# Kernel optimization log

Measured on AMD Instinct MI355X. Metric: run time of the kernel, lower is better.

Reference implementation:

```python
import jax, jax.numpy as jnp
import numpy as np

B_SZ, L, H, P = 4, 4096, 1024, 1024
R_MIN, R_MAX, MAX_PHASE = 0.0, 1.0, 6.28


def setup_inputs() -> dict:
    key = jax.random.key(0)
    ks = jax.random.split(key, 8)
    inputs = jax.random.normal(ks[0], (B_SZ, L, H), dtype=jnp.float32)
    # LRU-style init for nu_log/theta_log (keeps |lambda| < 1 so scan is stable)
    u1 = jax.random.uniform(ks[1], (P,))
    nu = -0.5 * jnp.log(u1 * (R_MAX**2 - R_MIN**2) + R_MIN**2)
    nu_log = jnp.log(nu)
    u2 = jax.random.uniform(ks[2], (P,))
    theta_log = jnp.log(MAX_PHASE * u2)
    # variance_scaling(0.5,'fan_out','normal') for B; (1.0,'fan_out','normal') for C
    B_re = jax.random.normal(ks[3], (P, H)) * jnp.sqrt(0.5 / P)
    B_im = jax.random.normal(ks[4], (P, H)) * jnp.sqrt(0.5 / P)
    C_re = jax.random.normal(ks[5], (H, P)) * jnp.sqrt(1.0 / H)
    C_im = jax.random.normal(ks[6], (H, P)) * jnp.sqrt(1.0 / H)
    D = jax.random.normal(ks[7], (H,))
    diag_lambda = jnp.exp(-jnp.exp(nu_log) + 1j * jnp.exp(theta_log))
    gamma_log = jnp.log(jnp.sqrt(1.0 - jnp.abs(diag_lambda) ** 2))
    return {
        "inputs": inputs,
        "nu_log": nu_log.astype(jnp.float32),
        "theta_log": theta_log.astype(jnp.float32),
        "B_re": B_re.astype(jnp.float32),
        "B_im": B_im.astype(jnp.float32),
        "C_re": C_re.astype(jnp.float32),
        "C_im": C_im.astype(jnp.float32),
        "D": D.astype(jnp.float32),
        "gamma_log": gamma_log.astype(jnp.float32),
    }


def reference(inputs, nu_log, theta_log, B_re, B_im, C_re, C_im, D, gamma_log):
    batch_size, input_length, _ = inputs.shape
    Lambda = jnp.exp(-jnp.exp(nu_log) + 1j * jnp.exp(theta_log))  # [P] complex
    Bmat = B_re + 1j * B_im                                        # [P,H]
    Cmat = C_re + 1j * C_im                                        # [H,P]
    gamma = jnp.exp(gamma_log)                                     # [P]
    B_norm = Bmat * gamma[:, None]

    def apply_step(elem_i, elem_j):
        a_i, bu_i = elem_i
        a_j, bu_j = elem_j
        return (a_j * a_i, a_j * bu_i + bu_j)

    Ls = jnp.broadcast_to(Lambda, (batch_size, input_length, Lambda.shape[0]))
    Bu = jnp.einsum('ph,blh->blp', B_norm, inputs.astype(B_norm.dtype))
    _, xs = jax.lax.associative_scan(apply_step, (Ls, Bu), axis=1)
    Cx = jnp.einsum('hp,blp->blh', Cmat, xs).real
    Du = D * inputs
    return Cx + Du
```

## Files before the change

kernel.cpp:

```cpp
#include <hip/hip_runtime.h>
#include <cstdint>
#include <cstddef>

#define MDIM 16384
#define HDIM 1024
#define PDIM 1024
#define LSEQ 4096
#define BSZ  4
#define CHUNK 64
#define NCHUNK 64
#define NBU  2048

typedef float   floatx4  __attribute__((ext_vector_type(4)));
typedef __bf16  bf16x8   __attribute__((ext_vector_type(8)));
typedef unsigned short u16;
typedef unsigned short u16x8 __attribute__((ext_vector_type(8)));

__device__ __forceinline__ u16 f2bf(float f) {
    union { float f; uint32_t u; } v; v.f = f;
    return (u16)((v.u + 0x7fffu + ((v.u >> 16) & 1u)) >> 16);
}
__device__ __forceinline__ float bfu2f(uint32_t bits16) {
    union { float f; uint32_t u; } v; v.u = bits16 << 16; return v.f;
}
__device__ __forceinline__ bf16x8 ldfrag(const u16* p) {
    return __builtin_bit_cast(bf16x8, *(const u16x8*)p);
}
__device__ __forceinline__ void gload16(const u16* g, u16* l) {
    __builtin_amdgcn_global_load_lds(
        (const __attribute__((address_space(1))) uint32_t*)g,
        (__attribute__((address_space(3))) uint32_t*)l, 16, 0, 0);
}

#define BARRIER() do { \
    asm volatile("" ::: "memory"); \
    __builtin_amdgcn_sched_barrier(0); \
    __builtin_amdgcn_s_barrier(); \
    __builtin_amdgcn_sched_barrier(0); \
    asm volatile("" ::: "memory"); \
} while (0)

#define WAITV(N_) do { \
    __builtin_amdgcn_sched_barrier(0); \
    asm volatile("s_waitcnt vmcnt(" #N_ ")" ::: "memory"); \
    __builtin_amdgcn_sched_barrier(0); \
} while (0)

template<int MH>
__device__ __forceinline__ void ldA(const u16* buf, int aBase, int c0, int c1,
                                    bf16x8 (&aF)[4][2]) {
    #pragma unroll
    for (int mf = 0; mf < 4; ++mf) {
        const u16* p = buf + aBase + (MH * 4 + mf) * 1024;
        aF[mf][0] = ldfrag(p + c0);
        aF[mf][1] = ldfrag(p + c1);
    }
}
template<int NH>
__device__ __forceinline__ void ldB(const u16* buf, int bBase, int c0, int c1,
                                    bf16x8 (&bF)[2][2]) {
    #pragma unroll
    for (int j = 0; j < 2; ++j) {
        const u16* p = buf + bBase + (NH * 2 + j) * 1024;
        bF[j][0] = ldfrag(p + c0);
        bF[j][1] = ldfrag(p + c1);
    }
}
template<int MH, int NH>
__device__ __forceinline__ void doMFMA(bf16x8 (&aF)[4][2], bf16x8 (&bF)[2][2],
                                       floatx4 (&acc)[8][4]) {
    __builtin_amdgcn_s_setprio(1);
    #pragma unroll
    for (int s = 0; s < 2; ++s)
        #pragma unroll
        for (int mf = 0; mf < 4; ++mf)
            #pragma unroll
            for (int j = 0; j < 2; ++j)
                acc[MH * 4 + mf][NH * 2 + j] =
                    __builtin_amdgcn_mfma_f32_16x16x32_bf16(
                        aF[mf][s], bF[j][s], acc[MH * 4 + mf][NH * 2 + j],
                        0, 0, 0);
    __builtin_amdgcn_s_setprio(0);
}

template<int KD>
__device__ __forceinline__ void gemm256_core(
    const u16* __restrict__ A, const u16* __restrict__ B,
    int m0, int n0, u16* smem, floatx4 (&acc)[8][4])
{
    const int tid  = threadIdx.x;
    const int wave = tid >> 6, lane = tid & 63;
    const int lrow = lane & 15, lq = lane >> 4;
    const int wm = wave >> 2, wn = wave & 3;
    const int axr = lrow & 7;
    const int c0 = (lq ^ axr) * 8;
    const int c1 = ((4 + lq) ^ axr) * 8;
    const int aBase = (wm * 128 + lrow) * 64;
    const int bBase = (wn * 64  + lrow) * 64;
    const int srow = tid >> 3;
    const int schk = (tid & 7) ^ (srow & 7);
    const u16* aptr = A + (size_t)(m0 + srow) * KD + schk * 8;
    const u16* bptr = B + (size_t)(n0 + srow) * KD + schk * 8;
    u16* const sA0 = smem;
    u16* const sB0 = smem + 16384;
    u16* const sA1 = smem + 32768;
    u16* const sB1 = smem + 49152;
    const int lw = wave * 512;

    bf16x8 aF[4][2], bF[2][2];

    #pragma unroll
    for (int i = 0; i < 4; ++i) {
        gload16(aptr + (size_t)i * 64 * KD, sA0 + i * 4096 + lw);
        gload16(bptr + (size_t)i * 64 * KD, sB0 + i * 4096 + lw);
    }
    WAITV(0);
    BARRIER();

    #define STG(i_, k_, dA_, dB_) do { \
        gload16(aptr + (size_t)(i_) * 64 * KD + (k_), (dA_) + (i_) * 4096 + lw); \
        gload16(bptr + (size_t)(i_) * 64 * KD + (k_), (dB_) + (i_) * 4096 + lw); \
    } while (0)

    for (int k = 0; k < KD; k += 128) {
        const int k1 = k + 64, k2 = k + 128;
        STG(0, k1, sA1, sB1);
        WAITV(2);
        BARRIER();
        ldA<0>(sA0, aBase, c0, c1, aF);
        ldB<0>(sB0, bBase, c0, c1, bF);
        doMFMA<0, 0>(aF, bF, acc);
        BARRIER();
        ldB<1>(sB0, bBase, c0, c1, bF);
        STG(1, k1, sA1, sB1);
        BARRIER();
        doMFMA<0, 1>(aF, bF, acc);
        BARRIER();
        ldA<1>(sA0, aBase, c0, c1, aF);
        STG(2, k1, sA1, sB1);
        BARRIER();
        doMFMA<1, 1>(aF, bF, acc);
        BARRIER();
        ldB<0>(sB0, bBase, c0, c1, bF);
        STG(3, k1, sA1, sB1);
        BARRIER();
        doMFMA<1, 0>(aF, bF, acc);
        BARRIER();

        if (k2 < KD) { STG(0, k2, sA0, sB0); WAITV(2); } else { WAITV(0); }
        BARRIER();
        ldA<0>(sA1, aBase, c0, c1, aF);
        ldB<0>(sB1, bBase, c0, c1, bF);
        doMFMA<0, 0>(aF, bF, acc);
        BARRIER();

        ldB<1>(sB1, bBase, c0, c1, bF);
        if (k2 < KD) STG(1, k2, sA0, sB0);
        BARRIER();
        doMFMA<0, 1>(aF, bF, acc);
        BARRIER();

        ldA<1>(sA1, aBase, c0, c1, aF);
        if (k2 < KD) STG(2, k2, sA0, sB0);
        BARRIER();
        doMFMA<1, 1>(aF, bF, acc);
        BARRIER();

        ldB<0>(sB1, bBase, c0, c1, bF);
        if (k2 < KD) STG(3, k2, sA0, sB0);
        BARRIER();
        doMFMA<1, 0>(aF, bF, acc);
        BARRIER();
    }
    #undef STG
}

__global__ __launch_bounds__(512, 2) void gemm_bu_k(
    const u16* __restrict__ A, const u16* __restrict__ B, u16* __restrict__ O)
{
    __shared__ __align__(16) u16 smem[65536];
    floatx4 acc[8][4] = {};
    const int d = blockIdx.x;
    const int xcd = d & 7, s = d >> 3;
    const int m0 = (xcd * 8 + (s >> 3)) * 256;
    const int n0 = (s & 7) * 256;
    gemm256_core<HDIM>(A, B, m0, n0, smem, acc);

    const int tid = threadIdx.x, wave = tid >> 6, lane = tid & 63;
    const int lrow = lane & 15, lq = lane >> 4;
    const int wm = wave >> 2, wn = wave & 3;
    u16* lwp = smem + wave * 4096;
    #pragma unroll
    for (int mh = 0; mh < 2; ++mh) {
        #pragma unroll
        for (int mfl = 0; mfl < 4; ++mfl)
            #pragma unroll
            for (int nf = 0; nf < 4; ++nf)
                #pragma unroll
                for (int r = 0; r < 4; ++r) {
                    int rowl = mfl * 16 + lq * 4 + r;
                    int cpos = (nf * 2 + (lrow >> 3)) ^ (rowl & 7);
                    lwp[rowl * 64 + cpos * 8 + (lrow & 7)] =
                        f2bf(acc[mh * 4 + mfl][nf][r]);
                }
        int grow = m0 + wm * 128 + mh * 64 + lane;
        #pragma unroll
        for (int j = 0; j < 8; ++j) {
            int cpos = j ^ (lane & 7);
            *(u16x8*)(O + (size_t)grow * NBU + n0 + wn * 64 + j * 8) =
                *(const u16x8*)(lwp + lane * 64 + cpos * 8);
        }
    }
}

__global__ __launch_bounds__(512, 2) void gemm_out_k(
    const u16* __restrict__ A, const u16* __restrict__ B,
    const float* __restrict__ Dv, const u16* __restrict__ Ubf,
    float* __restrict__ O)
{
    __shared__ __align__(16) u16 smem[65536];
    floatx4 acc[8][4] = {};
    const int d = blockIdx.x;
    const int xcd = d & 7, s = d >> 3;
    const int m0 = (xcd * 8 + (s >> 2)) * 256;
    const int n0 = (s & 3) * 256;
    gemm256_core<NBU>(A, B, m0, n0, smem, acc);

    const int tid = threadIdx.x, wave = tid >> 6, lane = tid & 63;
    const int lrow = lane & 15, lq = lane >> 4;
    const int wm = wave >> 2, wn = wave & 3;
    #pragma unroll
    for (int nf = 0; nf < 4; ++nf) {
        int col = n0 + wn * 64 + nf * 16 + lrow;
        float dval = Dv[col];
        #pragma unroll
        for (int mf = 0; mf < 8; ++mf)
            #pragma unroll
            for (int r = 0; r < 4; ++r) {
                int row = m0 + wm * 128 + mf * 16 + lq * 4 + r;
                size_t o = (size_t)row * HDIM + col;
                O[o] = acc[mf][nf][r] + dval * bfu2f(Ubf[o]);
            }
    }
}

__global__ __launch_bounds__(256) void prep_all(
    const float* __restrict__ U, u16* __restrict__ Ubf,
    const float* __restrict__ Bre, const float* __restrict__ Bim,
    const float* __restrict__ gamma_log, u16* __restrict__ Bcomb,
    const float* __restrict__ Cre, const float* __restrict__ Cim,
    u16* __restrict__ Bcbf)
{
    const int bid = blockIdx.x;
    if (bid < 8192) {
        size_t i = ((size_t)bid * 256 + threadIdx.x) * 8;
        float4 a = *(const float4*)(U + i);
        float4 b = *(const float4*)(U + i + 4);
        u16x8 w;
        w[0]=f2bf(a.x); w[1]=f2bf(a.y); w[2]=f2bf(a.z); w[3]=f2bf(a.w);
        w[4]=f2bf(b.x); w[5]=f2bf(b.y); w[6]=f2bf(b.z); w[7]=f2bf(b.w);
        *(u16x8*)(Ubf + i) = w;
    } else if (bid < 9216) {
        int t = (bid - 8192) * 256 + threadIdx.x;
        int n = t >> 7;
        int h = (t & 127) * 8;
        int p = n >> 1, sflag = n & 1;
        const float* src = (sflag ? Bim : Bre) + (size_t)p * HDIM + h;
        float g = expf(gamma_log[p]);
        float4 a = *(const float4*)src;
        float4 b = *(const float4*)(src + 4);
        u16x8 w;
        w[0]=f2bf(a.x*g); w[1]=f2bf(a.y*g); w[2]=f2bf(a.z*g); w[3]=f2bf(a.w*g);
        w[4]=f2bf(b.x*g); w[5]=f2bf(b.y*g); w[6]=f2bf(b.z*g); w[7]=f2bf(b.w*g);
        *(u16x8*)(Bcomb + (size_t)n * HDIM + h) = w;
    } else {
        int t = (bid - 9216) * 256 + threadIdx.x;
        int h = t >> 8;
        int k = (t & 255) * 4;
        float4 cr = *(const float4*)(Cre + (size_t)h * PDIM + k);
        float4 ci = *(const float4*)(Cim + (size_t)h * PDIM + k);
        u16x8 w;
        w[0]=f2bf(cr.x); w[1]=f2bf(-ci.x);
        w[2]=f2bf(cr.y); w[3]=f2bf(-ci.y);
        w[4]=f2bf(cr.z); w[5]=f2bf(-ci.z);
        w[6]=f2bf(cr.w); w[7]=f2bf(-ci.w);
        *(u16x8*)(Bcbf + (size_t)h * NBU + 2 * k) = w;
    }
}

__global__ __launch_bounds__(256) void scan_passA(
    const uint32_t* __restrict__ BuC,
    const float* __restrict__ nu_log, const float* __restrict__ theta_log,
    float* __restrict__ endC)
{
    int tid = blockIdx.x * 256 + threadIdx.x;
    int p0 = (tid & 511) * 2;
    int c  = (tid >> 9) & (NCHUNK - 1);
    int b  = tid >> 15;
    float nu0 = expf(nu_log[p0]),     th0 = expf(theta_log[p0]);
    float nu1 = expf(nu_log[p0 + 1]), th1 = expf(theta_log[p0 + 1]);
    float el0 = expf(-nu0), el1 = expf(-nu1);
    float lr0 = el0 * cosf(th0), li0 = el0 * sinf(th0);
    float lr1 = el1 * cosf(th1), li1 = el1 * sinf(th1);
    const uint32_t* src = BuC + (size_t)(b * LSEQ + c * CHUNK) * PDIM + p0;
    float xr0 = 0.f, xi0 = 0.f, xr1 = 0.f, xi1 = 0.f;
    #pragma unroll 8
    for (int t = 0; t < CHUNK; ++t) {
        uint2 v = *(const uint2*)(src + (size_t)t * PDIM);
        float br0 = bfu2f(v.x & 0xffffu), bi0 = bfu2f(v.x >> 16);
        float br1 = bfu2f(v.y & 0xffffu), bi1 = bfu2f(v.y >> 16);
        float nr0 = fmaf(lr0, xr0, fmaf(-li0, xi0, br0));
        float ni0 = fmaf(lr0, xi0, fmaf(li0, xr0, bi0));
        float nr1 = fmaf(lr1, xr1, fmaf(-li1, xi1, br1));
        float ni1 = fmaf(lr1, xi1, fmaf(li1, xr1, bi1));
        xr0 = nr0; xi0 = ni0; xr1 = nr1; xi1 = ni1;
    }
    float4 e; e.x = xr0; e.y = xi0; e.z = xr1; e.w = xi1;
    *(float4*)(endC + (((size_t)b * NCHUNK + c) * PDIM + p0) * 2) = e;
}

__global__ __launch_bounds__(256) void scan_passB(
    const float* __restrict__ endC,
    const float* __restrict__ nu_log, const float* __restrict__ theta_log,
    float* __restrict__ carryC)
{
    int tid = blockIdx.x * 256 + threadIdx.x;
    int p0 = (tid & 511) * 2;
    int b  = tid >> 9;
    float nu0 = expf(nu_log[p0]),     th0 = expf(theta_log[p0]);
    float nu1 = expf(nu_log[p0 + 1]), th1 = expf(theta_log[p0 + 1]);
    float e0 = expf(-nu0 * (float)CHUNK), a0 = th0 * (float)CHUNK;
    float e1 = expf(-nu1 * (float)CHUNK), a1 = th1 * (float)CHUNK;
    float Lr0 = e0 * cosf(a0), Li0 = e0 * sinf(a0);
    float Lr1 = e1 * cosf(a1), Li1 = e1 * sinf(a1);
    float gr0 = 0.f, gi0 = 0.f, gr1 = 0.f, gi1 = 0.f;
    for (int g = 0; g < 8; ++g) {
        float4 e[8];
        #pragma unroll
        for (int j = 0; j < 8; ++j)
            e[j] = *(const float4*)(endC + (((size_t)b * NCHUNK + g * 8 + j) * PDIM + p0) * 2);
        #pragma unroll
        for (int j = 0; j < 8; ++j) {
            size_t idx = (((size_t)b * NCHUNK + g * 8 + j) * PDIM + p0) * 2;
            float4 go; go.x = gr0; go.y = gi0; go.z = gr1; go.w = gi1;
            *(float4*)(carryC + idx) = go;
            float nr0 = fmaf(Lr0, gr0, fmaf(-Li0, gi0, e[j].x));
            float ni0 = fmaf(Lr0, gi0, fmaf(Li0, gr0, e[j].y));
            float nr1 = fmaf(Lr1, gr1, fmaf(-Li1, gi1, e[j].z));
            float ni1 = fmaf(Lr1, gi1, fmaf(Li1, gr1, e[j].w));
            gr0 = nr0; gi0 = ni0; gr1 = nr1; gi1 = ni1;
        }
    }
}

__global__ __launch_bounds__(256) void scan_passC(
    uint32_t* __restrict__ BuC,
    const float* __restrict__ nu_log, const float* __restrict__ theta_log,
    const float* __restrict__ carryC)
{
    int tid = blockIdx.x * 256 + threadIdx.x;
    int p0 = (tid & 511) * 2;
    int c  = (tid >> 9) & (NCHUNK - 1);
    int b  = tid >> 15;
    float nu0 = expf(nu_log[p0]),     th0 = expf(theta_log[p0]);
    float nu1 = expf(nu_log[p0 + 1]), th1 = expf(theta_log[p0 + 1]);
    float el0 = expf(-nu0), el1 = expf(-nu1);
    float lr0 = el0 * cosf(th0), li0 = el0 * sinf(th0);
    float lr1 = el1 * cosf(th1), li1 = el1 * sinf(th1);
    float4 g = *(const float4*)(carryC + (((size_t)b * NCHUNK + c) * PDIM + p0) * 2);
    float xr0 = g.x, xi0 = g.y, xr1 = g.z, xi1 = g.w;
    uint32_t* ptr = BuC + (size_t)(b * LSEQ + c * CHUNK) * PDIM + p0;
    #pragma unroll 8
    for (int t = 0; t < CHUNK; ++t) {
        uint32_t* q = ptr + (size_t)t * PDIM;
        uint2 v = *(const uint2*)q;
        float br0 = bfu2f(v.x & 0xffffu), bi0 = bfu2f(v.x >> 16);
        float br1 = bfu2f(v.y & 0xffffu), bi1 = bfu2f(v.y >> 16);
        float nr0 = fmaf(lr0, xr0, fmaf(-li0, xi0, br0));
        float ni0 = fmaf(lr0, xi0, fmaf(li0, xr0, bi0));
        float nr1 = fmaf(lr1, xr1, fmaf(-li1, xi1, br1));
        float ni1 = fmaf(lr1, xi1, fmaf(li1, xr1, bi1));
        xr0 = nr0; xi0 = ni0; xr1 = nr1; xi1 = ni1;
        uint2 o;
        o.x = (uint32_t)f2bf(xr0) | ((uint32_t)f2bf(xi0) << 16);
        o.y = (uint32_t)f2bf(xr1) | ((uint32_t)f2bf(xi1) << 16);
        *(uint2*)q = o;
    }
}

extern "C" void kernel_launch(void* const* d_in, const int* in_sizes, int n_in,
                              void* d_out, int out_size, void* d_ws, size_t ws_size,
                              hipStream_t stream)
{
    (void)in_sizes; (void)n_in; (void)out_size; (void)ws_size;
    const float* U         = (const float*)d_in[0];
    const float* nu_log    = (const float*)d_in[1];
    const float* theta_log = (const float*)d_in[2];
    const float* B_re      = (const float*)d_in[3];
    const float* B_im      = (const float*)d_in[4];
    const float* C_re      = (const float*)d_in[5];
    const float* C_im      = (const float*)d_in[6];
    const float* Dv        = (const float*)d_in[7];
    const float* gamma_log = (const float*)d_in[8];
    float* out = (float*)d_out;

    char* ws = (char*)d_ws;
    u16*   BuC    = (u16*)ws;
    u16*   Ubf    = (u16*)(ws + (size_t)64 * 1024 * 1024);
    u16*   Bcomb  = (u16*)(ws + (size_t)96 * 1024 * 1024);
    u16*   Bcbf   = (u16*)(ws + (size_t)100 * 1024 * 1024);
    float* endC   = (float*)(ws + (size_t)104 * 1024 * 1024);
    float* carryC = (float*)(ws + (size_t)106 * 1024 * 1024);

    prep_all<<<8192 + 1024 + 1024, 256, 0, stream>>>(
        U, Ubf, B_re, B_im, gamma_log, Bcomb, C_re, C_im, Bcbf);

    gemm_bu_k<<<512, 512, 0, stream>>>(Ubf, Bcomb, BuC);

    scan_passA<<<(BSZ * NCHUNK * PDIM / 2) / 256, 256, 0, stream>>>(
        (const uint32_t*)BuC, nu_log, theta_log, endC);
    scan_passB<<<(BSZ * PDIM / 2) / 256, 256, 0, stream>>>(endC, nu_log, theta_log, carryC);
    scan_passC<<<(BSZ * NCHUNK * PDIM / 2) / 256, 256, 0, stream>>>(
        (uint32_t*)BuC, nu_log, theta_log, carryC);

    gemm_out_k<<<256, 512, 0, stream>>>(BuC, Bcbf, Dv, Ubf, out);
}
```

Before: 352.9 us.

## Restructure GEMM main loop into ping-pong buffers with finer-grained staged loads

Replaces the unrolled two-stage k-loop in the 256x256 bf16 GEMM core with a single loop over 64-wide k tiles that swaps current and next shared-memory buffer pointers. Global-to-LDS staging is split into half-tile groups (B rows first, then A rows in an interleaved order), with partial vmcnt waits so the next tile's loads overlap more of the current tile's MFMAs. Both B fragment halves are kept in registers (bFa/bFb), so the redundant ldB<0> reload is dropped. This raises register pressure under the 512x2 launch bounds and depends on the reordered wait counts being correct.

```diff
diff --git a/kernel.cpp b/kernel.cpp
--- a/kernel.cpp
+++ b/kernel.cpp
@@ -101,78 +101,59 @@
     const int schk = (tid & 7) ^ (srow & 7);
     const u16* aptr = A + (size_t)(m0 + srow) * KD + schk * 8;
     const u16* bptr = B + (size_t)(n0 + srow) * KD + schk * 8;
-    u16* const sA0 = smem;
-    u16* const sB0 = smem + 16384;
-    u16* const sA1 = smem + 32768;
-    u16* const sB1 = smem + 49152;
     const int lw = wave * 512;
 
-    bf16x8 aF[4][2], bF[2][2];
-
-    #pragma unroll
-    for (int i = 0; i < 4; ++i) {
-        gload16(aptr + (size_t)i * 64 * KD, sA0 + i * 4096 + lw);
-        gload16(bptr + (size_t)i * 64 * KD, sB0 + i * 4096 + lw);
-    }
-    WAITV(0);
+    u16* curA = smem;          u16* curB = smem + 16384;
+    u16* nxtA = smem + 32768;  u16* nxtB = smem + 49152;
+
+    bf16x8 aF[4][2], bFa[2][2], bFb[2][2];
+
+    #define STG2(p_, d_, i0_, i1_, k_) do { \
+        gload16((p_) + (size_t)(i0_) * 64 * KD + (k_), (d_) + (i0_) * 4096 + lw); \
+        gload16((p_) + (size_t)(i1_) * 64 * KD + (k_), (d_) + (i1_) * 4096 + lw); \
+    } while (0)
+
+    STG2(bptr, curB, 0, 1, 0);
+    STG2(bptr, curB, 2, 3, 0);
+    STG2(aptr, curA, 0, 2, 0);
+    STG2(aptr, curA, 1, 3, 0);
+    WAITV(2);
     BARRIER();
 
-    #define STG(i_, k_, dA_, dB_) do { \
-        gload16(aptr + (size_t)(i_) * 64 * KD + (k_), (dA_) + (i_) * 4096 + lw); \
-        gload16(bptr + (size_t)(i_) * 64 * KD + (k_), (dB_) + (i_) * 4096 + lw); \
-    } while (0)
-
-    for (int k = 0; k < KD; k += 128) {
-        const int k1 = k + 64, k2 = k + 128;
-        STG(0, k1, sA1, sB1);
-        WAITV(2);
-        BARRIER();
-        ldA<0>(sA0, aBase, c0, c1, aF);
-        ldB<0>(sB0, bBase, c0, c1, bF);
-        doMFMA<0, 0>(aF, bF, acc);
-        BARRIER();
-        ldB<1>(sB0, bBase, c0, c1, bF);
-        STG(1, k1, sA1, sB1);
-        BARRIER();
-        doMFMA<0, 1>(aF, bF, acc);
-        BARRIER();
-        ldA<1>(sA0, aBase, c0, c1, aF);
-        STG(2, k1, sA1, sB1);
-        BARRIER();
-        doMFMA<1, 1>(aF, bF, acc);
-        BARRIER();
-        ldB<0>(sB0, bBase, c0, c1, bF);
-        STG(3, k1, sA1, sB1);
-        BARRIER();
-        doMFMA<1, 0>(aF, bF, acc);
-        BARRIER();
-
-        if (k2 < KD) { STG(0, k2, sA0, sB0); WAITV(2); } else { WAITV(0); }
-        BARRIER();
-        ldA<0>(sA1, aBase, c0, c1, aF);
-        ldB<0>(sB1, bBase, c0, c1, bF);
-        doMFMA<0, 0>(aF, bF, acc);
-        BARRIER();
-
-        ldB<1>(sB1, bBase, c0, c1, bF);
-        if (k2 < KD) STG(1, k2, sA0, sB0);
-        BARRIER();
-        doMFMA<0, 1>(aF, bF, acc);
-        BARRIER();
-
-        ldA<1>(sA1, aBase, c0, c1, aF);
-        if (k2 < KD) STG(2, k2, sA0, sB0);
-        BARRIER();
-        doMFMA<1, 1>(aF, bF, acc);
-        BARRIER();
-
-        ldB<0>(sB1, bBase, c0, c1, bF);
-        if (k2 < KD) STG(3, k2, sA0, sB0);
-        BARRIER();
-        doMFMA<1, 0>(aF, bF, acc);
-        BARRIER();
-    }
-    #undef STG
+    const int NT = KD / 64;
+    for (int t = 0; t < NT; ++t) {
+        const int kn = (t + 1) * 64;
+        const bool hn = (t + 1 < NT);
+
+        ldA<0>(curA, aBase, c0, c1, aF);
+        ldB<0>(curB, bBase, c0, c1, bFa);
+        if (hn) STG2(bptr, nxtB, 0, 1, kn);
+        BARRIER();
+        doMFMA<0, 0>(aF, bFa, acc);
+        BARRIER();
+
+        ldB<1>(curB, bBase, c0, c1, bFb);
+        if (hn) STG2(bptr, nxtB, 2, 3, kn);
+        BARRIER();
+        doMFMA<0, 1>(aF, bFb, acc);
+        if (hn) { WAITV(4); } else { WAITV(0); }
+        BARRIER();
+
+        ldA<1>(curA, aBase, c0, c1, aF);
+        if (hn) STG2(aptr, nxtA, 0, 2, kn);
+        BARRIER();
+        doMFMA<1, 1>(aF, bFb, acc);
+        BARRIER();
+
+        if (hn) STG2(aptr, nxtA, 1, 3, kn);
+        doMFMA<1, 0>(aF, bFa, acc);
+        if (hn) WAITV(2);
+        BARRIER();
+
+        u16* tA = curA; curA = nxtA; nxtA = tA;
+        u16* tB = curB; curB = nxtB; nxtB = tB;
+    }
+    #undef STG2
 }
 
 __global__ __launch_bounds__(512, 2) void gemm_bu_k(
```

Result: no change. 353.4 us (+0.1%).
